# Kernel tuning notes

Hardware: AMD Instinct MI355X
Metric: run time of the kernel (lower is better)

The kernel has to match this reference:

```python
import jax, jax.numpy as jnp
import numpy as np

N, K, D = 20000, 32, 128


def setup_inputs() -> dict:
    key = jax.random.key(0)
    ks = jax.random.split(key, 10)
    return {
        "self_feats": jax.random.normal(ks[0], (N, D), jnp.float32),
        "self_vecs": jax.random.normal(ks[1], (N, D), jnp.float32),
        "neigh_vecs": jax.random.normal(ks[2], (N, K, D), jnp.float32),
        "link_vecs": jax.random.normal(ks[3], (N, K, D), jnp.float32),
        # selection probabilities kept away from 0 to avoid huge 1/p values
        "select_probs": jax.random.uniform(ks[4], (N, K), jnp.float32, 0.1, 1.0),
        "gate_self_w": jax.random.normal(ks[5], (D,), jnp.float32) * (1.0 / np.sqrt(D)),
        "gate_neigh_w": jax.random.normal(ks[6], (D,), jnp.float32) * (1.0 / np.sqrt(D)),
        "gate_link_w": jax.random.normal(ks[7], (D,), jnp.float32) * (1.0 / np.sqrt(D)),
        "self_weights": jax.random.normal(ks[8], (D, D), jnp.float32) * (1.0 / np.sqrt(D)),
        "link_weights": jax.random.normal(ks[9], (D, D), jnp.float32) * (1.0 / np.sqrt(D)),
    }


def reference(self_feats, self_vecs, neigh_vecs, link_vecs, select_probs,
              gate_self_w, gate_neigh_w, gate_link_w, self_weights, link_weights):
    # Gate: scalar-per-(node, neighbor) sigmoid gate. dropout=0, no gate bias.
    trans_self = self_vecs @ gate_self_w                       # [N]
    trans_neigh = jnp.einsum('nkd,d->nk', neigh_vecs, gate_neigh_w)  # [N,K]
    trans_link = jnp.einsum('nkd,d->nk', link_vecs, gate_link_w)     # [N,K]
    gate = jax.nn.sigmoid(trans_self[:, None] + trans_neigh + trans_link)  # [N,K]

    # Link-conditioned channel amplification
    trans_links = jax.nn.sigmoid(jnp.einsum('nkd,de->nke', link_vecs, link_weights))  # [N,K,D]
    trans_self_feats = self_feats @ self_weights                                      # [N,D]

    amplified = neigh_vecs * trans_links * trans_self_feats[:, None, :]               # [N,K,D]

    # select_probs is not None branch: importance-weighted mean over neighbors
    gate_div_prob = gate / select_probs                                               # [N,K]
    sum_neighs = jnp.mean(amplified * gate_div_prob[..., None], axis=-2)              # [N,D]

    return jax.nn.relu(sum_neighs)
```

## Files before the change

### kernel.cpp

```cpp
#include <hip/hip_runtime.h>
#include <stdint.h>

#define N_NODES 20000
#define K_NB 32
#define D_DIM 128

typedef short bf16x8 __attribute__((ext_vector_type(8)));
typedef float f32x4 __attribute__((ext_vector_type(4)));

__device__ __forceinline__ unsigned short f2bf(float f) {
    union { float f; unsigned u; } v; v.f = f;
    unsigned r = v.u + 0x7FFFu + ((v.u >> 16) & 1u);
    return (unsigned short)(r >> 16);
}

__device__ __forceinline__ bf16x8 pack8(float4 a, float4 b) {
    bf16x8 r;
    r[0] = (short)f2bf(a.x); r[1] = (short)f2bf(a.y);
    r[2] = (short)f2bf(a.z); r[3] = (short)f2bf(a.w);
    r[4] = (short)f2bf(b.x); r[5] = (short)f2bf(b.y);
    r[6] = (short)f2bf(b.z); r[7] = (short)f2bf(b.w);
    return r;
}

__device__ __forceinline__ float dot16(float4 a0, float4 a1, float4 a2, float4 a3,
                                       float4 b0, float4 b1, float4 b2, float4 b3) {
    return a0.x*b0.x + a0.y*b0.y + a0.z*b0.z + a0.w*b0.w
         + a1.x*b1.x + a1.y*b1.y + a1.z*b1.z + a1.w*b1.w
         + a2.x*b2.x + a2.y*b2.y + a2.z*b2.z + a2.w*b2.w
         + a3.x*b3.x + a3.y*b3.y + a3.z*b3.z + a3.w*b3.w;
}

__device__ __forceinline__ float sigm(float x) {
    return __builtin_amdgcn_rcpf(1.0f + __expf(-x));
}

#define A_STRIDE 136
#define NG_STRIDE 132

__global__ __launch_bounds__(256) void precompute_kernel(
    const float* __restrict__ self_feats,
    const float* __restrict__ self_vecs,
    const float* __restrict__ gate_self_w,
    const float* __restrict__ self_weights,
    float* __restrict__ tsf,
    float* __restrict__ ts)
{
    __shared__ __align__(16) unsigned short A[32 * A_STRIDE];

    const int tid  = threadIdx.x;
    const int lane = tid & 63;
    const int w    = tid >> 6;
    const int q    = lane >> 4;
    const int el   = lane & 15;
    const int row  = tid >> 3;
    const int seg  = tid & 7;
    const int node0 = blockIdx.x * 32;

    bf16x8 wf[2][4];
#pragma unroll
    for (int nt = 0; nt < 2; ++nt) {
        int e = 32 * w + 16 * nt + el;
#pragma unroll
        for (int s = 0; s < 4; ++s) {
#pragma unroll
            for (int j = 0; j < 8; ++j) {
                int d = 32 * s + 8 * q + j;
                wf[nt][s][j] = (short)f2bf(self_weights[d * 128 + e]);
            }
        }
    }

    const float4* gs = (const float4*)(gate_self_w + seg * 16);
    float4 g0 = gs[0], g1 = gs[1], g2 = gs[2], g3 = gs[3];

    {
        const float4* sfr = (const float4*)(self_feats + (size_t)(node0 + row) * 128 + seg * 16);
        float4 v0 = sfr[0], v1 = sfr[1], v2 = sfr[2], v3 = sfr[3];
        const float4* svr = (const float4*)(self_vecs + (size_t)(node0 + row) * 128 + seg * 16);
        float4 u0 = svr[0], u1 = svr[1], u2 = svr[2], u3 = svr[3];

        float part = dot16(u0, u1, u2, u3, g0, g1, g2, g3);
        part += __shfl_xor(part, 1);
        part += __shfl_xor(part, 2);
        part += __shfl_xor(part, 4);
        if (seg == 0) ts[node0 + row] = part;

        *(bf16x8*)&A[row * A_STRIDE + seg * 16]     = pack8(v0, v1);
        *(bf16x8*)&A[row * A_STRIDE + seg * 16 + 8] = pack8(v2, v3);
    }
    __syncthreads();

    f32x4 acc[2][2] = {};
#pragma unroll
    for (int s = 0; s < 4; ++s) {
        bf16x8 a0 = *(const bf16x8*)&A[(el)      * A_STRIDE + 32 * s + 8 * q];
        bf16x8 a1 = *(const bf16x8*)&A[(16 + el) * A_STRIDE + 32 * s + 8 * q];
        acc[0][0] = __builtin_amdgcn_mfma_f32_16x16x32_bf16(a0, wf[0][s], acc[0][0], 0, 0, 0);
        acc[0][1] = __builtin_amdgcn_mfma_f32_16x16x32_bf16(a0, wf[1][s], acc[0][1], 0, 0, 0);
        acc[1][0] = __builtin_amdgcn_mfma_f32_16x16x32_bf16(a1, wf[0][s], acc[1][0], 0, 0, 0);
        acc[1][1] = __builtin_amdgcn_mfma_f32_16x16x32_bf16(a1, wf[1][s], acc[1][1], 0, 0, 0);
    }

#pragma unroll
    for (int mt = 0; mt < 2; ++mt)
#pragma unroll
        for (int nt = 0; nt < 2; ++nt)
#pragma unroll
            for (int r = 0; r < 4; ++r) {
                int m = 16 * mt + 4 * q + r;
                tsf[(size_t)(node0 + m) * 128 + 32 * w + 16 * nt + el] = acc[mt][nt][r];
            }
}

__global__ __launch_bounds__(256, 3) void aggregate_kernel(
    const float* __restrict__ neigh_vecs,
    const float* __restrict__ link_vecs,
    const float* __restrict__ select_probs,
    const float* __restrict__ gate_neigh_w,
    const float* __restrict__ gate_link_w,
    const float* __restrict__ link_weights,
    const float* __restrict__ tsf,
    const float* __restrict__ ts,
    float* __restrict__ out)
{
    __shared__ __align__(16) unsigned short A[32 * A_STRIDE];
    __shared__ __align__(16) float NG[32 * NG_STRIDE];
    __shared__ float t_s[32];
    __shared__ float sp_s[32];

    const int tid  = threadIdx.x;
    const int lane = tid & 63;
    const int w    = tid >> 6;
    const int q    = lane >> 4;
    const int el   = lane & 15;
    const int row  = tid >> 3;
    const int seg  = tid & 7;

    bf16x8 wf[2][4];
#pragma unroll
    for (int nt = 0; nt < 2; ++nt) {
        int e = 32 * w + 16 * nt + el;
#pragma unroll
        for (int s = 0; s < 4; ++s) {
#pragma unroll
            for (int j = 0; j < 8; ++j) {
                int d = 32 * s + 8 * q + j;
                wf[nt][s][j] = (short)f2bf(link_weights[d * 128 + e]);
            }
        }
    }

    const float4* glp = (const float4*)(gate_link_w + seg * 16);
    float4 gl0 = glp[0], gl1 = glp[1], gl2 = glp[2], gl3 = glp[3];
    const float4* gnp = (const float4*)(gate_neigh_w + seg * 16);
    float4 gn0 = gnp[0], gn1 = gnp[1], gn2 = gnp[2], gn3 = gnp[3];

    const int stride = gridDim.x;

    float4 v0, v1, v2, v3, u0, u1, u2, u3;
    float sp_r = 1.0f, ts_r = 0.0f, tsf_r0 = 0.0f, tsf_r1 = 0.0f;
    {
        int n = blockIdx.x;
        const float4* lr = (const float4*)(link_vecs + ((size_t)n * 32 + row) * 128 + seg * 16);
        v0 = lr[0]; v1 = lr[1]; v2 = lr[2]; v3 = lr[3];
        const float4* nr = (const float4*)(neigh_vecs + ((size_t)n * 32 + row) * 128 + seg * 16);
        u0 = nr[0]; u1 = nr[1]; u2 = nr[2]; u3 = nr[3];
        if (tid < 32) sp_r = select_probs[(size_t)n * 32 + tid];
        ts_r   = ts[n];
        tsf_r0 = tsf[(size_t)n * 128 + 32 * w + el];
        tsf_r1 = tsf[(size_t)n * 128 + 32 * w + 16 + el];
    }

    for (int n = blockIdx.x; n < N_NODES; n += stride) {
        float tl = dot16(v0, v1, v2, v3, gl0, gl1, gl2, gl3);
        tl += __shfl_xor(tl, 1);
        tl += __shfl_xor(tl, 2);
        tl += __shfl_xor(tl, 4);
        float tn = dot16(u0, u1, u2, u3, gn0, gn1, gn2, gn3);
        tn += __shfl_xor(tn, 1);
        tn += __shfl_xor(tn, 2);
        tn += __shfl_xor(tn, 4);
        if (seg == 0) t_s[row] = tl + tn;
        if (tid < 32) sp_s[tid] = __builtin_amdgcn_rcpf(32.0f * sp_r);

        *(bf16x8*)&A[row * A_STRIDE + seg * 16]     = pack8(v0, v1);
        *(bf16x8*)&A[row * A_STRIDE + seg * 16 + 8] = pack8(v2, v3);
        float4* ngp = (float4*)&NG[row * NG_STRIDE + seg * 16];
        ngp[0] = u0; ngp[1] = u1; ngp[2] = u2; ngp[3] = u3;

        float ts_cur = ts_r, tc0 = tsf_r0, tc1 = tsf_r1;

        __syncthreads();

        {
            int np = n + stride;
            np = (np < N_NODES) ? np : n;
            const float4* lr = (const float4*)(link_vecs + ((size_t)np * 32 + row) * 128 + seg * 16);
            v0 = lr[0]; v1 = lr[1]; v2 = lr[2]; v3 = lr[3];
            const float4* nr = (const float4*)(neigh_vecs + ((size_t)np * 32 + row) * 128 + seg * 16);
            u0 = nr[0]; u1 = nr[1]; u2 = nr[2]; u3 = nr[3];
            if (tid < 32) sp_r = select_probs[(size_t)np * 32 + tid];
            ts_r   = ts[np];
            tsf_r0 = tsf[(size_t)np * 128 + 32 * w + el];
            tsf_r1 = tsf[(size_t)np * 128 + 32 * w + 16 + el];
        }

        f32x4 acc[2][2] = {};
#pragma unroll
        for (int s = 0; s < 4; ++s) {
            bf16x8 a0 = *(const bf16x8*)&A[(el)      * A_STRIDE + 32 * s + 8 * q];
            bf16x8 a1 = *(const bf16x8*)&A[(16 + el) * A_STRIDE + 32 * s + 8 * q];
            acc[0][0] = __builtin_amdgcn_mfma_f32_16x16x32_bf16(a0, wf[0][s], acc[0][0], 0, 0, 0);
            acc[0][1] = __builtin_amdgcn_mfma_f32_16x16x32_bf16(a0, wf[1][s], acc[0][1], 0, 0, 0);
            acc[1][0] = __builtin_amdgcn_mfma_f32_16x16x32_bf16(a1, wf[0][s], acc[1][0], 0, 0, 0);
            acc[1][1] = __builtin_amdgcn_mfma_f32_16x16x32_bf16(a1, wf[1][s], acc[1][1], 0, 0, 0);
        }

        float g[2][4];
#pragma unroll
        for (int mt = 0; mt < 2; ++mt)
#pragma unroll
            for (int r = 0; r < 4; ++r) {
                int m = 16 * mt + 4 * q + r;
                g[mt][r] = sigm(ts_cur + t_s[m]) * sp_s[m];
            }

#pragma unroll
        for (int nt = 0; nt < 2; ++nt) {
            int c0 = 32 * w + 16 * nt;
            float s = 0.0f;
#pragma unroll
            for (int mt = 0; mt < 2; ++mt)
#pragma unroll
                for (int r = 0; r < 4; ++r) {
                    int m = 16 * mt + 4 * q + r;
                    float t = sigm(acc[mt][nt][r]);
                    s += t * NG[m * NG_STRIDE + c0 + el] * g[mt][r];
                }
            s += __shfl_xor(s, 16);
            s += __shfl_xor(s, 32);
            if (q == 0) {
                float tc = nt == 0 ? tc0 : tc1;
                float o = tc * s;
                out[(size_t)n * 128 + c0 + el] = o > 0.0f ? o : 0.0f;
            }
        }

        __syncthreads();
    }
}

extern "C" void kernel_launch(void* const* d_in, const int* in_sizes, int n_in,
                              void* d_out, int out_size, void* d_ws, size_t ws_size,
                              hipStream_t stream) {
    const float* self_feats   = (const float*)d_in[0];
    const float* self_vecs    = (const float*)d_in[1];
    const float* neigh_vecs   = (const float*)d_in[2];
    const float* link_vecs    = (const float*)d_in[3];
    const float* select_probs = (const float*)d_in[4];
    const float* gate_self_w  = (const float*)d_in[5];
    const float* gate_neigh_w = (const float*)d_in[6];
    const float* gate_link_w  = (const float*)d_in[7];
    const float* self_weights = (const float*)d_in[8];
    const float* link_weights = (const float*)d_in[9];
    float* out = (float*)d_out;

    float* tsf = (float*)d_ws;
    float* ts  = tsf + (size_t)N_NODES * D_DIM;

    precompute_kernel<<<N_NODES / 32, 256, 0, stream>>>(
        self_feats, self_vecs, gate_self_w, self_weights, tsf, ts);
    aggregate_kernel<<<2048, 256, 0, stream>>>(
        neigh_vecs, link_vecs, select_probs, gate_neigh_w, gate_link_w,
        link_weights, tsf, ts, out);
}
```

Baseline: 661.9 us.

## Double-buffer node prefetch two iterations ahead and fold gate into neighbor staging

```diff
diff --git a/kernel.cpp b/kernel.cpp
--- a/kernel.cpp
+++ b/kernel.cpp
@@ -33,6 +33,10 @@
 
 __device__ __forceinline__ float sigm(float x) {
     return __builtin_amdgcn_rcpf(1.0f + __expf(-x));
+}
+
+__device__ __forceinline__ float4 scale4(float4 a, float s) {
+    float4 r; r.x = a.x*s; r.y = a.y*s; r.z = a.z*s; r.w = a.w*s; return r;
 }
 
 #define A_STRIDE 136
@@ -113,7 +117,96 @@
             }
 }
 
-__global__ __launch_bounds__(256, 3) void aggregate_kernel(
+struct Pref {
+    float4 v0, v1, v2, v3;
+    float4 u0, u1, u2, u3;
+    float sp, ts, t0, t1;
+};
+
+__device__ __forceinline__ void load_node(
+    Pref& P, int n, int row, int seg, int w, int el,
+    const float* __restrict__ link_vecs, const float* __restrict__ neigh_vecs,
+    const float* __restrict__ select_probs, const float* __restrict__ ts,
+    const float* __restrict__ tsf)
+{
+    const float4* lr = (const float4*)(link_vecs + ((size_t)n * 32 + row) * 128 + seg * 16);
+    P.v0 = lr[0]; P.v1 = lr[1]; P.v2 = lr[2]; P.v3 = lr[3];
+    const float4* nr = (const float4*)(neigh_vecs + ((size_t)n * 32 + row) * 128 + seg * 16);
+    P.u0 = nr[0]; P.u1 = nr[1]; P.u2 = nr[2]; P.u3 = nr[3];
+    P.sp = select_probs[(size_t)n * 32 + row];
+    P.ts = ts[n];
+    P.t0 = tsf[(size_t)n * 128 + 32 * w + el];
+    P.t1 = tsf[(size_t)n * 128 + 32 * w + 16 + el];
+}
+
+__device__ __forceinline__ void process_node(
+    Pref& P, int n_cur, int n_next,
+    int row, int seg, int w, int q, int el,
+    unsigned short* A, float* NG,
+    const bf16x8 (&wf)[2][4],
+    float4 gl0, float4 gl1, float4 gl2, float4 gl3,
+    float4 gn0, float4 gn1, float4 gn2, float4 gn3,
+    const float* __restrict__ link_vecs, const float* __restrict__ neigh_vecs,
+    const float* __restrict__ select_probs, const float* __restrict__ ts,
+    const float* __restrict__ tsf, float* __restrict__ out)
+{
+    float tl = dot16(P.v0, P.v1, P.v2, P.v3, gl0, gl1, gl2, gl3);
+    tl += __shfl_xor(tl, 1);
+    tl += __shfl_xor(tl, 2);
+    tl += __shfl_xor(tl, 4);
+    float tn = dot16(P.u0, P.u1, P.u2, P.u3, gn0, gn1, gn2, gn3);
+    tn += __shfl_xor(tn, 1);
+    tn += __shfl_xor(tn, 2);
+    tn += __shfl_xor(tn, 4);
+    float g_row = sigm(P.ts + tl + tn) * __builtin_amdgcn_rcpf(32.0f * P.sp);
+
+    *(bf16x8*)&A[row * A_STRIDE + seg * 16]     = pack8(P.v0, P.v1);
+    *(bf16x8*)&A[row * A_STRIDE + seg * 16 + 8] = pack8(P.v2, P.v3);
+    float4* ngp = (float4*)&NG[row * NG_STRIDE + seg * 16];
+    ngp[0] = scale4(P.u0, g_row); ngp[1] = scale4(P.u1, g_row);
+    ngp[2] = scale4(P.u2, g_row); ngp[3] = scale4(P.u3, g_row);
+
+    float tc0 = P.t0, tc1 = P.t1;
+
+    __syncthreads();
+
+    load_node(P, n_next, row, seg, w, el, link_vecs, neigh_vecs, select_probs, ts, tsf);
+
+    f32x4 acc[2][2] = {};
+#pragma unroll
+    for (int s = 0; s < 4; ++s) {
+        bf16x8 a0 = *(const bf16x8*)&A[(el)      * A_STRIDE + 32 * s + 8 * q];
+        bf16x8 a1 = *(const bf16x8*)&A[(16 + el) * A_STRIDE + 32 * s + 8 * q];
+        acc[0][0] = __builtin_amdgcn_mfma_f32_16x16x32_bf16(a0, wf[0][s], acc[0][0], 0, 0, 0);
+        acc[0][1] = __builtin_amdgcn_mfma_f32_16x16x32_bf16(a0, wf[1][s], acc[0][1], 0, 0, 0);
+        acc[1][0] = __builtin_amdgcn_mfma_f32_16x16x32_bf16(a1, wf[0][s], acc[1][0], 0, 0, 0);
+        acc[1][1] = __builtin_amdgcn_mfma_f32_16x16x32_bf16(a1, wf[1][s], acc[1][1], 0, 0, 0);
+    }
+
+#pragma unroll
+    for (int nt = 0; nt < 2; ++nt) {
+        int c0 = 32 * w + 16 * nt;
+        float s = 0.0f;
+#pragma unroll
+        for (int mt = 0; mt < 2; ++mt)
+#pragma unroll
+            for (int r = 0; r < 4; ++r) {
+                int m = 16 * mt + 4 * q + r;
+                s += sigm(acc[mt][nt][r]) * NG[m * NG_STRIDE + c0 + el];
+            }
+        s += __shfl_xor(s, 16);
+        s += __shfl_xor(s, 32);
+        if (q == 0) {
+            float tc = nt == 0 ? tc0 : tc1;
+            float o = tc * s;
+            out[(size_t)n_cur * 128 + c0 + el] = o > 0.0f ? o : 0.0f;
+        }
+    }
+
+    __syncthreads();
+}
+
+__global__ __launch_bounds__(256, 2) void aggregate_kernel(
     const float* __restrict__ neigh_vecs,
     const float* __restrict__ link_vecs,
     const float* __restrict__ select_probs,
@@ -126,8 +219,6 @@
 {
     __shared__ __align__(16) unsigned short A[32 * A_STRIDE];
     __shared__ __align__(16) float NG[32 * NG_STRIDE];
-    __shared__ float t_s[32];
-    __shared__ float sp_s[32];
 
     const int tid  = threadIdx.x;
     const int lane = tid & 63;
@@ -158,96 +249,29 @@
 
     const int stride = gridDim.x;
 
-    float4 v0, v1, v2, v3, u0, u1, u2, u3;
-    float sp_r = 1.0f, ts_r = 0.0f, tsf_r0 = 0.0f, tsf_r1 = 0.0f;
+    Pref PA, PB;
+    int n = blockIdx.x;
+    load_node(PA, n, row, seg, w, el, link_vecs, neigh_vecs, select_probs, ts, tsf);
     {
-        int n = blockIdx.x;
-        const float4* lr = (const float4*)(link_vecs + ((size_t)n * 32 + row) * 128 + seg * 16);
-        v0 = lr[0]; v1 = lr[1]; v2 = lr[2]; v3 = lr[3];
-        const float4* nr = (const float4*)(neigh_vecs + ((size_t)n * 32 + row) * 128 + seg * 16);
-        u0 = nr[0]; u1 = nr[1]; u2 = nr[2]; u3 = nr[3];
-        if (tid < 32) sp_r = select_probs[(size_t)n * 32 + tid];
-        ts_r   = ts[n];
-        tsf_r0 = tsf[(size_t)n * 128 + 32 * w + el];
-        tsf_r1 = tsf[(size_t)n * 128 + 32 * w + 16 + el];
-    }
-
-    for (int n = blockIdx.x; n < N_NODES; n += stride) {
-        float tl = dot16(v0, v1, v2, v3, gl0, gl1, gl2, gl3);
-        tl += __shfl_xor(tl, 1);
-        tl += __shfl_xor(tl, 2);
-        tl += __shfl_xor(tl, 4);
-        float tn = dot16(u0, u1, u2, u3, gn0, gn1, gn2, gn3);
-        tn += __shfl_xor(tn, 1);
-        tn += __shfl_xor(tn, 2);
-        tn += __shfl_xor(tn, 4);
-        if (seg == 0) t_s[row] = tl + tn;
-        if (tid < 32) sp_s[tid] = __builtin_amdgcn_rcpf(32.0f * sp_r);
-
-        *(bf16x8*)&A[row * A_STRIDE + seg * 16]     = pack8(v0, v1);
-        *(bf16x8*)&A[row * A_STRIDE + seg * 16 + 8] = pack8(v2, v3);
-        float4* ngp = (float4*)&NG[row * NG_STRIDE + seg * 16];
-        ngp[0] = u0; ngp[1] = u1; ngp[2] = u2; ngp[3] = u3;
-
-        float ts_cur = ts_r, tc0 = tsf_r0, tc1 = tsf_r1;
-
-        __syncthreads();
-
-        {
-            int np = n + stride;
-            np = (np < N_NODES) ? np : n;
-            const float4* lr = (const float4*)(link_vecs + ((size_t)np * 32 + row) * 128 + seg * 16);
-            v0 = lr[0]; v1 = lr[1]; v2 = lr[2]; v3 = lr[3];
-            const float4* nr = (const float4*)(neigh_vecs + ((size_t)np * 32 + row) * 128 + seg * 16);
-            u0 = nr[0]; u1 = nr[1]; u2 = nr[2]; u3 = nr[3];
-            if (tid < 32) sp_r = select_probs[(size_t)np * 32 + tid];
-            ts_r   = ts[np];
-            tsf_r0 = tsf[(size_t)np * 128 + 32 * w + el];
-            tsf_r1 = tsf[(size_t)np * 128 + 32 * w + 16 + el];
-        }
-
-        f32x4 acc[2][2] = {};
-#pragma unroll
-        for (int s = 0; s < 4; ++s) {
-            bf16x8 a0 = *(const bf16x8*)&A[(el)      * A_STRIDE + 32 * s + 8 * q];
-            bf16x8 a1 = *(const bf16x8*)&A[(16 + el) * A_STRIDE + 32 * s + 8 * q];
-            acc[0][0] = __builtin_amdgcn_mfma_f32_16x16x32_bf16(a0, wf[0][s], acc[0][0], 0, 0, 0);
-            acc[0][1] = __builtin_amdgcn_mfma_f32_16x16x32_bf16(a0, wf[1][s], acc[0][1], 0, 0, 0);
-            acc[1][0] = __builtin_amdgcn_mfma_f32_16x16x32_bf16(a1, wf[0][s], acc[1][0], 0, 0, 0);
-            acc[1][1] = __builtin_amdgcn_mfma_f32_16x16x32_bf16(a1, wf[1][s], acc[1][1], 0, 0, 0);
-        }
-
-        float g[2][4];
-#pragma unroll
-        for (int mt = 0; mt < 2; ++mt)
-#pragma unroll
-            for (int r = 0; r < 4; ++r) {
-                int m = 16 * mt + 4 * q + r;
-                g[mt][r] = sigm(ts_cur + t_s[m]) * sp_s[m];
-            }
-
-#pragma unroll
-        for (int nt = 0; nt < 2; ++nt) {
-            int c0 = 32 * w + 16 * nt;
-            float s = 0.0f;
-#pragma unroll
-            for (int mt = 0; mt < 2; ++mt)
-#pragma unroll
-                for (int r = 0; r < 4; ++r) {
-                    int m = 16 * mt + 4 * q + r;
-                    float t = sigm(acc[mt][nt][r]);
-                    s += t * NG[m * NG_STRIDE + c0 + el] * g[mt][r];
-                }
-            s += __shfl_xor(s, 16);
-            s += __shfl_xor(s, 32);
-            if (q == 0) {
-                float tc = nt == 0 ? tc0 : tc1;
-                float o = tc * s;
-                out[(size_t)n * 128 + c0 + el] = o > 0.0f ? o : 0.0f;
-            }
-        }
-
-        __syncthreads();
+        int n1 = n + stride;
+        load_node(PB, (n1 < N_NODES) ? n1 : n, row, seg, w, el,
+                  link_vecs, neigh_vecs, select_probs, ts, tsf);
+    }
+
+    for (;;) {
+        int n2 = n + 2 * stride;
+        process_node(PA, n, (n2 < N_NODES) ? n2 : n, row, seg, w, q, el,
+                     A, NG, wf, gl0, gl1, gl2, gl3, gn0, gn1, gn2, gn3,
+                     link_vecs, neigh_vecs, select_probs, ts, tsf, out);
+        n += stride;
+        if (n >= N_NODES) break;
+
+        n2 = n + 2 * stride;
+        process_node(PB, n, (n2 < N_NODES) ? n2 : n, row, seg, w, q, el,
+                     A, NG, wf, gl0, gl1, gl2, gl3, gn0, gn1, gn2, gn3,
+                     link_vecs, neigh_vecs, select_probs, ts, tsf, out);
+        n += stride;
+        if (n >= N_NODES) break;
     }
 }
 
```

New measurement: 661.0 us. No clear change (-0.1%).
